# Optimization experiments

Hardware: AMD Instinct MI355X
Metric: run time of the kernel (lower is better)

Reference implementation:

```python
import jax, jax.numpy as jnp
import numpy as np

N, E, D_IN, D_H, D_OUT = 50000, 600000, 128, 128, 1


def setup_inputs() -> dict:
    key = jax.random.key(0)
    ks = jax.random.split(key, 12)
    s = 1.0 / np.sqrt(D_H)
    inp = {
        "x": jax.random.normal(ks[0], (N, D_IN), dtype=jnp.float32),
        "edge_index": jax.random.randint(ks[1], (2, E), 0, N, dtype=jnp.int64),
        # GCNConv layer weights (in->h, h->h, h->h)
        "W0": jax.random.normal(ks[2], (D_IN, D_H), dtype=jnp.float32) * s,
        "b0": jnp.zeros((D_H,), dtype=jnp.float32),
        "W1": jax.random.normal(ks[3], (D_H, D_H), dtype=jnp.float32) * s,
        "b1": jnp.zeros((D_H,), dtype=jnp.float32),
        "W2": jax.random.normal(ks[4], (D_H, D_H), dtype=jnp.float32) * s,
        "b2": jnp.zeros((D_H,), dtype=jnp.float32),
        # MLP head
        "mlp_w1": jax.random.normal(ks[5], (D_H, D_H), dtype=jnp.float32) * s,
        "mlp_b1": jnp.zeros((D_H,), dtype=jnp.float32),
        "mlp_w2": jax.random.normal(ks[6], (D_H, D_OUT), dtype=jnp.float32) * s,
        "mlp_b2": jnp.zeros((D_OUT,), dtype=jnp.float32),
    }
    return inp


def reference(x, edge_index, W0, b0, W1, b1, W2, b2, mlp_w1, mlp_b1, mlp_w2, mlp_b2):
    n = x.shape[0]
    loop = jnp.arange(n, dtype=edge_index.dtype)
    # add self-loops (PyG GCNConv default)
    src = jnp.concatenate([edge_index[0], loop])
    dst = jnp.concatenate([edge_index[1], loop])
    # symmetric normalization: deg counts incoming edges incl. self-loop
    deg = jax.ops.segment_sum(jnp.ones(src.shape, dtype=x.dtype), dst, num_segments=n)
    dinv = jax.lax.rsqrt(deg)  # deg >= 1 due to self-loops
    norm = (dinv[src] * dinv[dst])[:, None]  # [E+N, 1]

    def gcn_conv(h, W, b):
        h = h @ W                       # [N, d]
        msg = h[src] * norm             # gather + scale, [E+N, d]
        return jax.ops.segment_sum(msg, dst, num_segments=n) + b

    # num_layers=3: first two convs with ReLU (dropout is identity in eval)
    h = jax.nn.relu(gcn_conv(x, W0, b0))
    h = jax.nn.relu(gcn_conv(h, W1, b1))
    h = gcn_conv(h, W2, b2)
    # MLP head (dropout identity in eval)
    h = jax.nn.relu(h @ mlp_w1 + mlp_b1)
    return h @ mlp_w2 + mlp_b2
```

## Files before the change

### kernel.cpp

```cpp
#include <hip/hip_runtime.h>
#include <hip/hip_fp16.h>

constexpr int D = 128;

typedef _Float16 half8 __attribute__((ext_vector_type(8)));
typedef float f32x4 __attribute__((ext_vector_type(4)));


__global__ void k_zero(int4* __restrict__ p, int n4) {
    int i = blockIdx.x * 256 + threadIdx.x;
    if (i < n4) p[i] = make_int4(0, 0, 0, 0);
}


__global__ void k_count(const int* __restrict__ dst, int* __restrict__ cnt, int E) {
    int e = blockIdx.x * 256 + threadIdx.x;
    if (e < E) atomicAdd(&cnt[dst[e]], 1);
}

__global__ __launch_bounds__(256) void k_deg_stats(const int* __restrict__ cnt,
                                                   float* __restrict__ dinv,
                                                   int* __restrict__ bsum, int n) {
    __shared__ int sm[256];
    int tid = threadIdx.x;
    int i = blockIdx.x * 256 + tid;
    int c = (i < n) ? cnt[i] : 0;
    if (i < n) dinv[i] = rsqrtf((float)(c + 1));
    sm[tid] = c;
    __syncthreads();
    for (int off = 128; off > 0; off >>= 1) {
        if (tid < off) sm[tid] += sm[tid + off];
        __syncthreads();
    }
    if (tid == 0) bsum[blockIdx.x] = sm[0];
}

__global__ __launch_bounds__(256) void k_local_scan2(const int* __restrict__ cnt,
                                                     const int* __restrict__ bsum, int nb,
                                                     int* __restrict__ rowptr,
                                                     int* __restrict__ cursor, int n) {
    __shared__ int sb[256];
    __shared__ int sm[256];
    int tid = threadIdx.x;
    int bid = blockIdx.x;
    int bv = (tid < nb) ? bsum[tid] : 0;
    sb[tid] = bv;
    __syncthreads();
    for (int off = 1; off < 256; off <<= 1) {
        int t = (tid >= off) ? sb[tid - off] : 0;
        __syncthreads();
        sb[tid] += t;
        __syncthreads();
    }
    int blockoff = (bid > 0) ? sb[bid - 1] : 0;
    int i = bid * 256 + tid;
    int v = (i < n) ? cnt[i] : 0;
    sm[tid] = v;
    __syncthreads();
    for (int off = 1; off < 256; off <<= 1) {
        int t = (tid >= off) ? sm[tid - off] : 0;
        __syncthreads();
        sm[tid] += t;
        __syncthreads();
    }
    if (i < n) {
        int rp = blockoff + sm[tid] - v;
        rowptr[i] = rp;
        cursor[i] = rp;
    }
    if (bid == 0 && tid == 0) rowptr[n] = sb[nb - 1];
}


template <typename IdxT>
__global__ __launch_bounds__(256) void k_prep(
    const int* __restrict__ src, const int* __restrict__ dst, int* __restrict__ cursor,
    IdxT* __restrict__ csr, int E, const float* __restrict__ x,
    const float* __restrict__ dinv, __half* __restrict__ xh, int n4,
    const float* __restrict__ W0, const float* __restrict__ W1,
    const float* __restrict__ W2, const float* __restrict__ M1,
    const float* __restrict__ b2, const float* __restrict__ c1,
    __half* __restrict__ Wf0, __half* __restrict__ Wf1, __half* __restrict__ Wfp,
    float* __restrict__ cp) {
    int T = gridDim.x * 256;
    int gid = blockIdx.x * 256 + threadIdx.x;

    for (int e = gid; e < E; e += T) {
        int s = src[e], d = dst[e];
        int p = atomicAdd(&cursor[d], 1);
        csr[p] = (IdxT)s;
    }

    for (int i = gid; i < n4; i += T) {
        float4 v = reinterpret_cast<const float4*>(x)[i];
        float dd = dinv[i >> 5];
        __half ho[4] = {__float2half(v.x * dd), __float2half(v.y * dd),
                        __float2half(v.z * dd), __float2half(v.w * dd)};
        reinterpret_cast<uint2*>(xh)[i] = *reinterpret_cast<uint2*>(ho);
    }

    for (int q = gid; q < 2 * 16384; q += T) {
        int m = q >> 14;
        int idx = q & 16383;
        int j = idx & 7;
        int l = (idx >> 3) & 63;
        int c = (idx >> 9) & 7;
        int kk = (idx >> 12) & 3;
        int row = kk * 32 + (l >> 4) * 8 + j;
        int col = c * 16 + (l & 15);
        const float* W = (m == 0) ? W0 : W1;
        __half* Wf = (m == 0) ? Wf0 : Wf1;
        Wf[idx] = __float2half(W[row * 128 + col]);
    }

    for (int idx = gid; idx < 16384; idx += T) {
        int j = idx & 7;
        int l = (idx >> 3) & 63;
        int c = (idx >> 9) & 7;
        int kk = (idx >> 12) & 3;
        int row = kk * 32 + (l >> 4) * 8 + j;
        int col = c * 16 + (l & 15);
        float acc = 0.f;
        for (int k = 0; k < 128; ++k)
            acc = fmaf(W2[row * 128 + k], M1[k * 128 + col], acc);
        Wfp[idx] = __float2half(acc);
    }

    if (gid < 128) {
        float acc = c1[gid];
        for (int k = 0; k < 128; ++k) acc = fmaf(b2[k], M1[k * 128 + gid], acc);
        cp[gid] = acc;
    }
}


__device__ inline void accm(float* a, uint4 g, float m) {
    float2 p0 = __half22float2(*reinterpret_cast<const __half2*>(&g.x));
    float2 p1 = __half22float2(*reinterpret_cast<const __half2*>(&g.y));
    float2 p2 = __half22float2(*reinterpret_cast<const __half2*>(&g.z));
    float2 p3 = __half22float2(*reinterpret_cast<const __half2*>(&g.w));
    a[0] = fmaf(m, p0.x, a[0]);
    a[1] = fmaf(m, p0.y, a[1]);
    a[2] = fmaf(m, p1.x, a[2]);
    a[3] = fmaf(m, p1.y, a[3]);
    a[4] = fmaf(m, p2.x, a[4]);
    a[5] = fmaf(m, p2.y, a[5]);
    a[6] = fmaf(m, p3.x, a[6]);
    a[7] = fmaf(m, p3.y, a[7]);
}

template <int MODE, typename IdxT>
__global__ __launch_bounds__(256) void k_fused(const uint4* __restrict__ Ah4,
                                               const int* __restrict__ rowptr,
                                               const IdxT* __restrict__ csr,
                                               const float* __restrict__ dinv,
                                               const __half* __restrict__ Wf,
                                               const float* __restrict__ bias,
                                               const float* __restrict__ m2,
                                               const float* __restrict__ m2b,
                                               void* __restrict__ outv, int n) {
    __shared__ uint4 Ht[32 * 16];
    __shared__ float ph[2][32];
    int tid = threadIdx.x;
    int wv = tid >> 6;
    int lane = tid & 63;
    int r0 = blockIdx.x * 32;

    int half = lane >> 5;
    int l31 = lane & 31;
    int qg2 = (lane >> 4) & 1;
    int fl = lane & 15;
    for (int it = 0; it < 4; ++it) {
        int lr = wv * 8 + it * 2 + half;
        int i = r0 + lr;
        if (i >= n) i = n - 1;
        float a[8];
#pragma unroll
        for (int j = 0; j < 8; ++j) a[j] = 0.f;
        int beg = rowptr[i], end = rowptr[i + 1];
        for (int base = beg; base < end; base += 32) {
            int c2 = end - base;
            if (c2 > 32) c2 = 32;
            int idxv = (base + l31 < end) ? (int)csr[base + l31] : 0;
            for (int e = 0; e < c2; e += 8) {
                int k0 = e + qg2;
                int k1 = e + qg2 + 2;
                int k2 = e + qg2 + 4;
                int k3 = e + qg2 + 6;
                int s0 = __shfl(idxv, half * 32 + k0);
                int s1 = __shfl(idxv, half * 32 + k1);
                int s2 = __shfl(idxv, half * 32 + k2);
                int s3 = __shfl(idxv, half * 32 + k3);
                uint4 g0 = Ah4[s0 * 16 + fl];
                uint4 g1 = Ah4[s1 * 16 + fl];
                uint4 g2 = Ah4[s2 * 16 + fl];
                uint4 g3 = Ah4[s3 * 16 + fl];
                float m0 = (k0 < c2) ? 1.f : 0.f;
                float m1 = (k1 < c2) ? 1.f : 0.f;
                float m2_ = (k2 < c2) ? 1.f : 0.f;
                float m3 = (k3 < c2) ? 1.f : 0.f;
                accm(a, g0, m0);
                accm(a, g1, m1);
                accm(a, g2, m2_);
                accm(a, g3, m3);
            }
        }
#pragma unroll
        for (int j = 0; j < 8; ++j) a[j] += __shfl_xor(a[j], 16);
        if (qg2 == 0) {
            uint4 gs = Ah4[i * 16 + fl];
            accm(a, gs, 1.f);
            float di = dinv[i];
            __half ho[8];
#pragma unroll
            for (int j = 0; j < 8; ++j) ho[j] = __float2half(di * a[j]);
            Ht[lr * 16 + (fl ^ (lr & 7))] = *reinterpret_cast<const uint4*>(ho);
        }
    }
    __syncthreads();

    int w4 = wv & 1;
    int ch = wv >> 1;
    int rr = w4 * 16 + (lane & 15);

    f32x4 acc[4];
#pragma unroll
    for (int c = 0; c < 4; ++c) acc[c] = (f32x4){0.f, 0.f, 0.f, 0.f};

#pragma unroll
    for (int kk = 0; kk < 4; ++kk) {
        int bk = kk * 4 + (lane >> 4);
        half8 a = *reinterpret_cast<const half8*>(&Ht[rr * 16 + (bk ^ (rr & 7))]);
#pragma unroll
        for (int c = 0; c < 4; ++c) {
            int gc = ch * 4 + c;
            half8 b = *reinterpret_cast<const half8*>(&Wf[((kk * 8 + gc) * 64 + lane) * 8]);
            acc[c] = __builtin_amdgcn_mfma_f32_16x16x32_f16(a, b, acc[c], 0, 0, 0);
        }
    }

    float bv[4];
#pragma unroll
    for (int c = 0; c < 4; ++c) bv[c] = bias[ch * 64 + c * 16 + (lane & 15)];

    if (MODE == 0) {
        __half* outh = (__half*)outv;
#pragma unroll
        for (int reg = 0; reg < 4; ++reg) {
            int r = r0 + w4 * 16 + (lane >> 4) * 4 + reg;
            if (r < n) {
                float dr = dinv[r];
#pragma unroll
                for (int c = 0; c < 4; ++c) {
                    float v = dr * fmaxf(acc[c][reg] + bv[c], 0.f);
                    outh[r * 128 + ch * 64 + c * 16 + (lane & 15)] = __float2half(v);
                }
            }
        }
    } else {
        float* out = (float*)outv;
        float mv[4];
#pragma unroll
        for (int c = 0; c < 4; ++c) mv[c] = m2[ch * 64 + c * 16 + (lane & 15)];
#pragma unroll
        for (int reg = 0; reg < 4; ++reg) {
            float p = 0.f;
#pragma unroll
            for (int c = 0; c < 4; ++c)
                p = fmaf(fmaxf(acc[c][reg] + bv[c], 0.f), mv[c], p);
            p += __shfl_xor(p, 1);
            p += __shfl_xor(p, 2);
            p += __shfl_xor(p, 4);
            p += __shfl_xor(p, 8);
            if ((lane & 15) == 0) ph[ch][w4 * 16 + (lane >> 4) * 4 + reg] = p;
        }
        __syncthreads();
        if (tid < 32) {
            int r = r0 + tid;
            if (r < n) out[r] = ph[0][tid] + ph[1][tid] + m2b[0];
        }
    }
}


extern "C" void kernel_launch(void* const* d_in, const int* in_sizes, int n_in,
                              void* d_out, int out_size, void* d_ws, size_t ws_size,
                              hipStream_t stream) {
    const float* x = (const float*)d_in[0];
    const int* ei = (const int*)d_in[1];
    const float* W0 = (const float*)d_in[2];
    const float* b0 = (const float*)d_in[3];
    const float* W1 = (const float*)d_in[4];
    const float* b1 = (const float*)d_in[5];
    const float* W2 = (const float*)d_in[6];
    const float* b2 = (const float*)d_in[7];
    const float* M1 = (const float*)d_in[8];
    const float* c1 = (const float*)d_in[9];
    const float* m2 = (const float*)d_in[10];
    const float* m2b = (const float*)d_in[11];
    float* out = (float*)d_out;

    int N = in_sizes[0] / D;
    int E = in_sizes[1] / 2;
    const int* src = ei;
    const int* dst = ei + E;

    char* ws = (char*)d_ws;
    size_t off = 0;
    auto alloc = [&](size_t bytes) -> void* {
        void* p = ws + off;
        off += (bytes + 255) & ~(size_t)255;
        return p;
    };

    int gN = (N + 255) / 256;
    int gFused = (N + 31) / 32;
    int nElem4 = N * D / 4;

    __half* xh = (__half*)alloc((size_t)N * D * 2);
    __half* bufA = (__half*)alloc((size_t)N * D * 2);
    __half* bufB = (__half*)alloc((size_t)N * D * 2);
    int* cnt = (int*)alloc((size_t)N * 4);
    float* dinv = (float*)alloc((size_t)N * 4);
    int* rowptr = (int*)alloc((size_t)(N + 1) * 4);
    int* cursor = (int*)alloc((size_t)N * 4);
    void* csr = alloc((size_t)E * 4);
    float* cp = (float*)alloc((size_t)D * 4);
    __half* Wf0 = (__half*)alloc((size_t)D * D * 2);
    __half* Wf1 = (__half*)alloc((size_t)D * D * 2);
    __half* Wfp = (__half*)alloc((size_t)D * D * 2);
    int* bsum = (int*)alloc((size_t)gN * 4);

    bool small_idx = (N <= 65535);

    int zc = (N + 3) / 4;
    k_zero<<<(zc + 255) / 256, 256, 0, stream>>>((int4*)cnt, zc);
    k_count<<<(E + 255) / 256, 256, 0, stream>>>(dst, cnt, E);
    k_deg_stats<<<gN, 256, 0, stream>>>(cnt, dinv, bsum, N);
    k_local_scan2<<<gN, 256, 0, stream>>>(cnt, bsum, gN, rowptr, cursor, N);
    if (small_idx)
        k_prep<ushort><<<2048, 256, 0, stream>>>(src, dst, cursor, (ushort*)csr, E, x,
                                                 dinv, xh, nElem4, W0, W1, W2, M1, b2,
                                                 c1, Wf0, Wf1, Wfp, cp);
    else
        k_prep<uint><<<2048, 256, 0, stream>>>(src, dst, cursor, (uint*)csr, E, x, dinv,
                                               xh, nElem4, W0, W1, W2, M1, b2, c1, Wf0,
                                               Wf1, Wfp, cp);

    auto fused0 = [&](const __half* in_h, const __half* Wf, const float* b,
                      __half* out_h) {
        if (small_idx)
            k_fused<0, ushort><<<gFused, 256, 0, stream>>>(
                (const uint4*)in_h, rowptr, (const ushort*)csr, dinv, Wf, b, nullptr,
                nullptr, out_h, N);
        else
            k_fused<0, uint><<<gFused, 256, 0, stream>>>(
                (const uint4*)in_h, rowptr, (const uint*)csr, dinv, Wf, b, nullptr,
                nullptr, out_h, N);
    };

    fused0(xh, Wf0, b0, bufA);
    fused0(bufA, Wf1, b1, bufB);
    if (small_idx)
        k_fused<1, ushort><<<gFused, 256, 0, stream>>>(
            (const uint4*)bufB, rowptr, (const ushort*)csr, dinv, Wfp, cp, m2, m2b, out,
            N);
    else
        k_fused<1, uint><<<gFused, 256, 0, stream>>>(
            (const uint4*)bufB, rowptr, (const uint*)csr, dinv, Wfp, cp, m2, m2b, out,
            N);
}
```

Before: 172.1 us.

## Merge graph-build preprocessing kernels into one cooperative kernel with grid syncs

Replaces the zero, count, degree-stats, scan and prep launches with one cooperative kernel of 1024 blocks. Grid-wide syncs separate the phases, and the weight preprocessing now overlaps the count zeroing in the first phase. The aim is to remove several kernel launch gaps. In exchange it adds grid.sync costs, runs with fewer blocks than the previous 2048-block prep, and needs all 1024 blocks to be co-resident for a cooperative launch.

```diff
diff --git a/kernel.cpp b/kernel.cpp
--- a/kernel.cpp
+++ b/kernel.cpp
@@ -1,5 +1,8 @@
 #include <hip/hip_runtime.h>
 #include <hip/hip_fp16.h>
+#include <hip/hip_cooperative_groups.h>
+
+namespace cg = cooperative_groups;
 
 constexpr int D = 128;
 
@@ -7,98 +10,26 @@
 typedef float f32x4 __attribute__((ext_vector_type(4)));
 
 
-__global__ void k_zero(int4* __restrict__ p, int n4) {
-    int i = blockIdx.x * 256 + threadIdx.x;
-    if (i < n4) p[i] = make_int4(0, 0, 0, 0);
-}
-
-
-__global__ void k_count(const int* __restrict__ dst, int* __restrict__ cnt, int E) {
-    int e = blockIdx.x * 256 + threadIdx.x;
-    if (e < E) atomicAdd(&cnt[dst[e]], 1);
-}
-
-__global__ __launch_bounds__(256) void k_deg_stats(const int* __restrict__ cnt,
-                                                   float* __restrict__ dinv,
-                                                   int* __restrict__ bsum, int n) {
-    __shared__ int sm[256];
-    int tid = threadIdx.x;
-    int i = blockIdx.x * 256 + tid;
-    int c = (i < n) ? cnt[i] : 0;
-    if (i < n) dinv[i] = rsqrtf((float)(c + 1));
-    sm[tid] = c;
-    __syncthreads();
-    for (int off = 128; off > 0; off >>= 1) {
-        if (tid < off) sm[tid] += sm[tid + off];
-        __syncthreads();
-    }
-    if (tid == 0) bsum[blockIdx.x] = sm[0];
-}
-
-__global__ __launch_bounds__(256) void k_local_scan2(const int* __restrict__ cnt,
-                                                     const int* __restrict__ bsum, int nb,
-                                                     int* __restrict__ rowptr,
-                                                     int* __restrict__ cursor, int n) {
-    __shared__ int sb[256];
-    __shared__ int sm[256];
-    int tid = threadIdx.x;
-    int bid = blockIdx.x;
-    int bv = (tid < nb) ? bsum[tid] : 0;
-    sb[tid] = bv;
-    __syncthreads();
-    for (int off = 1; off < 256; off <<= 1) {
-        int t = (tid >= off) ? sb[tid - off] : 0;
-        __syncthreads();
-        sb[tid] += t;
-        __syncthreads();
-    }
-    int blockoff = (bid > 0) ? sb[bid - 1] : 0;
-    int i = bid * 256 + tid;
-    int v = (i < n) ? cnt[i] : 0;
-    sm[tid] = v;
-    __syncthreads();
-    for (int off = 1; off < 256; off <<= 1) {
-        int t = (tid >= off) ? sm[tid - off] : 0;
-        __syncthreads();
-        sm[tid] += t;
-        __syncthreads();
-    }
-    if (i < n) {
-        int rp = blockoff + sm[tid] - v;
-        rowptr[i] = rp;
-        cursor[i] = rp;
-    }
-    if (bid == 0 && tid == 0) rowptr[n] = sb[nb - 1];
-}
-
-
 template <typename IdxT>
-__global__ __launch_bounds__(256) void k_prep(
-    const int* __restrict__ src, const int* __restrict__ dst, int* __restrict__ cursor,
-    IdxT* __restrict__ csr, int E, const float* __restrict__ x,
-    const float* __restrict__ dinv, __half* __restrict__ xh, int n4,
+__global__ __launch_bounds__(256) void k_build(
+    const int* __restrict__ src, const int* __restrict__ dst, int E, int n, int gN,
+    int* __restrict__ cnt, float* __restrict__ dinv, int* __restrict__ bsum,
+    int* __restrict__ rowptr, int* __restrict__ cursor, IdxT* __restrict__ csr,
+    const float* __restrict__ x, __half* __restrict__ xh, int n4,
     const float* __restrict__ W0, const float* __restrict__ W1,
     const float* __restrict__ W2, const float* __restrict__ M1,
     const float* __restrict__ b2, const float* __restrict__ c1,
     __half* __restrict__ Wf0, __half* __restrict__ Wf1, __half* __restrict__ Wfp,
     float* __restrict__ cp) {
+    __shared__ int sb[256];
+    __shared__ int sm[256];
+    cg::grid_group grid = cg::this_grid();
+    int tid = threadIdx.x;
+    int bid = blockIdx.x;
     int T = gridDim.x * 256;
-    int gid = blockIdx.x * 256 + threadIdx.x;
-
-    for (int e = gid; e < E; e += T) {
-        int s = src[e], d = dst[e];
-        int p = atomicAdd(&cursor[d], 1);
-        csr[p] = (IdxT)s;
-    }
-
-    for (int i = gid; i < n4; i += T) {
-        float4 v = reinterpret_cast<const float4*>(x)[i];
-        float dd = dinv[i >> 5];
-        __half ho[4] = {__float2half(v.x * dd), __float2half(v.y * dd),
-                        __float2half(v.z * dd), __float2half(v.w * dd)};
-        reinterpret_cast<uint2*>(xh)[i] = *reinterpret_cast<uint2*>(ho);
-    }
-
+    int gid = bid * 256 + tid;
+
+    for (int i = gid; i < n; i += T) cnt[i] = 0;
     for (int q = gid; q < 2 * 16384; q += T) {
         int m = q >> 14;
         int idx = q & 16383;
@@ -112,7 +43,6 @@
         __half* Wf = (m == 0) ? Wf0 : Wf1;
         Wf[idx] = __float2half(W[row * 128 + col]);
     }
-
     for (int idx = gid; idx < 16384; idx += T) {
         int j = idx & 7;
         int l = (idx >> 3) & 63;
@@ -125,11 +55,70 @@
             acc = fmaf(W2[row * 128 + k], M1[k * 128 + col], acc);
         Wfp[idx] = __float2half(acc);
     }
-
     if (gid < 128) {
         float acc = c1[gid];
         for (int k = 0; k < 128; ++k) acc = fmaf(b2[k], M1[k * 128 + gid], acc);
         cp[gid] = acc;
+    }
+    grid.sync();
+
+    for (int e = gid; e < E; e += T) atomicAdd(&cnt[dst[e]], 1);
+    grid.sync();
+
+    for (int i = gid; i < n; i += T) dinv[i] = rsqrtf((float)(cnt[i] + 1));
+    if (bid < gN) {
+        int i = bid * 256 + tid;
+        sm[tid] = (i < n) ? cnt[i] : 0;
+        __syncthreads();
+        for (int off = 128; off > 0; off >>= 1) {
+            if (tid < off) sm[tid] += sm[tid + off];
+            __syncthreads();
+        }
+        if (tid == 0) bsum[bid] = sm[0];
+    }
+    grid.sync();
+
+    if (bid < gN) {
+        int bv = (tid < gN) ? bsum[tid] : 0;
+        sb[tid] = bv;
+        __syncthreads();
+        for (int off = 1; off < 256; off <<= 1) {
+            int t = (tid >= off) ? sb[tid - off] : 0;
+            __syncthreads();
+            sb[tid] += t;
+            __syncthreads();
+        }
+        int blockoff = (bid > 0) ? sb[bid - 1] : 0;
+        int i = bid * 256 + tid;
+        int v = (i < n) ? cnt[i] : 0;
+        sm[tid] = v;
+        __syncthreads();
+        for (int off = 1; off < 256; off <<= 1) {
+            int t = (tid >= off) ? sm[tid - off] : 0;
+            __syncthreads();
+            sm[tid] += t;
+            __syncthreads();
+        }
+        if (i < n) {
+            int rp = blockoff + sm[tid] - v;
+            rowptr[i] = rp;
+            cursor[i] = rp;
+        }
+        if (bid == 0 && tid == 0) rowptr[n] = sb[gN - 1];
+    }
+    grid.sync();
+
+    for (int e = gid; e < E; e += T) {
+        int s = src[e], d = dst[e];
+        int p = atomicAdd(&cursor[d], 1);
+        csr[p] = (IdxT)s;
+    }
+    for (int i = gid; i < n4; i += T) {
+        float4 v = reinterpret_cast<const float4*>(x)[i];
+        float dd = dinv[i >> 5];
+        __half ho[4] = {__float2half(v.x * dd), __float2half(v.y * dd),
+                        __float2half(v.z * dd), __float2half(v.w * dd)};
+        reinterpret_cast<uint2*>(xh)[i] = *reinterpret_cast<uint2*>(ho);
     }
 }
 
@@ -333,19 +322,28 @@
 
     bool small_idx = (N <= 65535);
 
-    int zc = (N + 3) / 4;
-    k_zero<<<(zc + 255) / 256, 256, 0, stream>>>((int4*)cnt, zc);
-    k_count<<<(E + 255) / 256, 256, 0, stream>>>(dst, cnt, E);
-    k_deg_stats<<<gN, 256, 0, stream>>>(cnt, dinv, bsum, N);
-    k_local_scan2<<<gN, 256, 0, stream>>>(cnt, bsum, gN, rowptr, cursor, N);
-    if (small_idx)
-        k_prep<ushort><<<2048, 256, 0, stream>>>(src, dst, cursor, (ushort*)csr, E, x,
-                                                 dinv, xh, nElem4, W0, W1, W2, M1, b2,
-                                                 c1, Wf0, Wf1, Wfp, cp);
-    else
-        k_prep<uint><<<2048, 256, 0, stream>>>(src, dst, cursor, (uint*)csr, E, x, dinv,
-                                               xh, nElem4, W0, W1, W2, M1, b2, c1, Wf0,
-                                               Wf1, Wfp, cp);
+    {
+        ushort* csr_s = (ushort*)csr;
+        uint* csr_u = (uint*)csr;
+        void* args_s[] = {(void*)&src,  (void*)&dst,  (void*)&E,     (void*)&N,
+                          (void*)&gN,   (void*)&cnt,  (void*)&dinv,  (void*)&bsum,
+                          (void*)&rowptr, (void*)&cursor, (void*)&csr_s, (void*)&x,
+                          (void*)&xh,   (void*)&nElem4, (void*)&W0,  (void*)&W1,
+                          (void*)&W2,   (void*)&M1,   (void*)&b2,    (void*)&c1,
+                          (void*)&Wf0,  (void*)&Wf1,  (void*)&Wfp,   (void*)&cp};
+        void* args_u[] = {(void*)&src,  (void*)&dst,  (void*)&E,     (void*)&N,
+                          (void*)&gN,   (void*)&cnt,  (void*)&dinv,  (void*)&bsum,
+                          (void*)&rowptr, (void*)&cursor, (void*)&csr_u, (void*)&x,
+                          (void*)&xh,   (void*)&nElem4, (void*)&W0,  (void*)&W1,
+                          (void*)&W2,   (void*)&M1,   (void*)&b2,    (void*)&c1,
+                          (void*)&Wf0,  (void*)&Wf1,  (void*)&Wfp,   (void*)&cp};
+        if (small_idx)
+            hipLaunchCooperativeKernel((const void*)k_build<ushort>, dim3(1024),
+                                       dim3(256), args_s, 0, stream);
+        else
+            hipLaunchCooperativeKernel((const void*)k_build<uint>, dim3(1024),
+                                       dim3(256), args_u, 0, stream);
+    }
 
     auto fused0 = [&](const __half* in_h, const __half* Wf, const float* b,
                       __half* out_h) {
```

New measurement: 597.2 us. +247.0%, slower.
